# Performance work log

Hardware: AMD Instinct MI355X
Metric: run time of the kernel (lower is better)

Reference implementation:

```python
import jax, jax.numpy as jnp
import numpy as np

B, D, H, T = 256, 1024, 1024, 100
EPS = 1e-5  # torch LayerNorm default

def _ln(x, g, b):
    m = jnp.mean(x, axis=-1, keepdims=True)
    v = jnp.mean((x - m) ** 2, axis=-1, keepdims=True)
    return (x - m) * jax.lax.rsqrt(v + EPS) * g + b

def _gru_cell(x, h, Wih, Whh, bih, bhh):
    # PyTorch GRUCell math. Wih:[3H,in], Whh:[3H,H], gate order r,z,n.
    gi = x @ Wih.T + bih
    gh = h @ Whh.T + bhh
    ir, iz, inn = jnp.split(gi, 3, axis=-1)
    hr, hz, hn = jnp.split(gh, 3, axis=-1)
    r = jax.nn.sigmoid(ir + hr)
    z = jax.nn.sigmoid(iz + hz)
    n = jnp.tanh(inn + r * hn)
    return (1.0 - z) * n + z * h

def setup_inputs() -> dict:
    key = jax.random.key(0)
    ks = jax.random.split(key, 16)
    def xav(k, shape):
        fan_out, fan_in = shape
        lim = np.sqrt(6.0 / (fan_in + fan_out))
        return jax.random.uniform(k, shape, jnp.float32, -lim, lim)
    inp = {
        'x': jax.random.normal(ks[0], (B, D), jnp.float32),
        'enc_W1': xav(ks[1], (H, D)), 'enc_b1': jnp.zeros((H,), jnp.float32),
        'enc_ln1_g': jnp.ones((H,), jnp.float32), 'enc_ln1_b': jnp.zeros((H,), jnp.float32),
        'enc_W2': xav(ks[2], (H, H)), 'enc_b2': jnp.zeros((H,), jnp.float32),
        'enc_ln2_g': jnp.ones((H,), jnp.float32), 'enc_ln2_b': jnp.zeros((H,), jnp.float32),
        'gru_Wih0': jax.random.uniform(ks[3], (3 * H, H), jnp.float32, -1/np.sqrt(H), 1/np.sqrt(H)),
        'gru_Whh0': jax.random.uniform(ks[4], (3 * H, H), jnp.float32, -1/np.sqrt(H), 1/np.sqrt(H)),
        'gru_bih0': jnp.zeros((3 * H,), jnp.float32), 'gru_bhh0': jnp.zeros((3 * H,), jnp.float32),
        'gru_Wih1': jax.random.uniform(ks[5], (3 * H, H), jnp.float32, -1/np.sqrt(H), 1/np.sqrt(H)),
        'gru_Whh1': jax.random.uniform(ks[6], (3 * H, H), jnp.float32, -1/np.sqrt(H), 1/np.sqrt(H)),
        'gru_bih1': jnp.zeros((3 * H,), jnp.float32), 'gru_bhh1': jnp.zeros((3 * H,), jnp.float32),
        'hn_g': jnp.ones((H,), jnp.float32), 'hn_b': jnp.zeros((H,), jnp.float32),
        'proj_W1': xav(ks[7], (H, H)), 'proj_b1': jnp.zeros((H,), jnp.float32),
        'proj_ln_g': jnp.ones((H,), jnp.float32), 'proj_ln_b': jnp.zeros((H,), jnp.float32),
        'proj_W2': xav(ks[8], (D, H)), 'proj_b2': jnp.zeros((D,), jnp.float32),
        'max_length': T,
    }
    return inp

def reference(x, enc_W1, enc_b1, enc_ln1_g, enc_ln1_b, enc_W2, enc_b2, enc_ln2_g, enc_ln2_b,
              gru_Wih0, gru_Whh0, gru_bih0, gru_bhh0, gru_Wih1, gru_Whh1, gru_bih1, gru_bhh1,
              hn_g, hn_b, proj_W1, proj_b1, proj_ln_g, proj_ln_b, proj_W2, proj_b2, max_length):
    # Encoder: Linear -> LN -> ReLU, twice
    e = jax.nn.relu(_ln(x @ enc_W1.T + enc_b1, enc_ln1_g, enc_ln1_b))
    e = jax.nn.relu(_ln(e @ enc_W2.T + enc_b2, enc_ln2_g, enc_ln2_b))
    h_init = jnp.zeros((2, x.shape[0], gru_Whh0.shape[1]), x.dtype)  # [num_layers,B,H]

    def step(carry, _):
        h, cur = carry
        hn = _ln(h, hn_g, hn_b)  # hidden_norm applied to h0 each step
        h0 = _gru_cell(cur, hn[0], gru_Wih0, gru_Whh0, gru_bih0, gru_bhh0)
        h1 = _gru_cell(h0, hn[1], gru_Wih1, gru_Whh1, gru_bih1, gru_bhh1)
        return (jnp.stack([h0, h1]), h1), h1

    (_, _), ys = jax.lax.scan(step, (h_init, e), None, length=max_length)
    outputs = jnp.transpose(ys, (1, 0, 2))  # [B,T,H]
    p = jax.nn.relu(_ln(outputs @ proj_W1.T + proj_b1, proj_ln_g, proj_ln_b))
    return p @ proj_W2.T + proj_b2  # [B,T,D]
```

## Files before the change

kernel.cpp:

```cpp
#include <hip/hip_runtime.h>
#include <stdint.h>

#define T_STEPS 100
#define Bb 256
#define Hh 1024
#define Dd 1024
#define BM 64
#define BN 64
#define BK 64

typedef _Float16 f16;
typedef _Float16 f16x8 __attribute__((ext_vector_type(8)));
typedef _Float16 f16x4 __attribute__((ext_vector_type(4)));
typedef float    f32x4 __attribute__((ext_vector_type(4)));

__global__ __launch_bounds__(256) void k_f32_split(const float* __restrict__ s,
                                                   f16* __restrict__ hi, f16* __restrict__ lo, int n) {
  int i = (blockIdx.x * blockDim.x + threadIdx.x) * 4;
  if (i >= n) return;
  float4 v = *(const float4*)(s + i);
  f16x4 h = { (f16)v.x, (f16)v.y, (f16)v.z, (f16)v.w };
  f16x4 L = { (f16)(v.x - (float)h.x), (f16)(v.y - (float)h.y),
              (f16)(v.z - (float)h.z), (f16)(v.w - (float)h.w) };
  *(f16x4*)(hi + i) = h;
  *(f16x4*)(lo + i) = L;
}

__global__ __launch_bounds__(256) void k_f32_to_f16(const float* __restrict__ s,
                                                    f16* __restrict__ d, int n) {
  int i = (blockIdx.x * blockDim.x + threadIdx.x) * 4;
  if (i >= n) return;
  float4 v = *(const float4*)(s + i);
  f16x4 o = { (f16)v.x, (f16)v.y, (f16)v.z, (f16)v.w };
  *(f16x4*)(d + i) = o;
}

__global__ __launch_bounds__(256) void k_init_hn(const float* __restrict__ lnb,
                                                 float* __restrict__ hn0f, float* __restrict__ hn1f,
                                                 f16* __restrict__ h0hi, f16* __restrict__ h0lo,
                                                 f16* __restrict__ h1hi, f16* __restrict__ h1lo) {
  int m = blockIdx.x, tid = threadIdx.x;
  for (int k = 0; k < 4; ++k) {
    int c = tid + k * 256;
    float v = lnb[c];
    f16 h = (f16)v; f16 L = (f16)(v - (float)h);
    size_t idx = (size_t)m * Hh + c;
    hn0f[idx] = v; hn1f[idx] = v;
    h0hi[idx] = h; h0lo[idx] = L;
    h1hi[idx] = h; h1lo[idx] = L;
  }
}

template <int NCH>
__device__ __forceinline__ void stage_rows(const f16* __restrict__ g, int r0, int k0,
                                           f16* sdst, int tid) {
#pragma unroll
  for (int i = 0; i < NCH; ++i) {
    int slot = i * 256 + tid;
    int row  = slot >> 3;
    int pkg  = slot & 7;
    int lg   = pkg ^ (row & 7);
    const f16* src = g + (size_t)(r0 + row) * 1024 + k0 + lg * 8;
    f16* dst = sdst + (size_t)slot * 8;
    __builtin_amdgcn_global_load_lds((const __attribute__((address_space(1))) void*)src,
                                     (__attribute__((address_space(3))) void*)dst, 16, 0, 0);
  }
}

#define FBM 64
#define FBN 96
__global__ __launch_bounds__(256) void k_gru_gemm(
    const f16* __restrict__ A0h, const f16* __restrict__ A0l,
    const f16* __restrict__ B0h, const f16* __restrict__ B0l, float* __restrict__ C0,
    const f16* __restrict__ A1h, const f16* __restrict__ A1l,
    const f16* __restrict__ B1h, const f16* __restrict__ B1l, float* __restrict__ C1) {
  const int wgid = blockIdx.x;
  const int xcd = wgid & 7, idx = wgid >> 3;
  const int bx = idx & 3, yp = (idx >> 2) & 3, bz = idx >> 4;
  const int by = xcd * 4 + yp;

  const f16* Ah = bz ? A1h : A0h;
  const f16* Al = bz ? A1l : A0l;
  const f16* Bh = bz ? B1h : B0h;
  const f16* Bl = bz ? B1l : B0l;
  float*     C  = bz ? C1  : C0;

  __shared__ alignas(16) f16 sAh[3][FBM * BK];
  __shared__ alignas(16) f16 sAl[3][FBM * BK];
  __shared__ alignas(16) f16 sBh[3][FBN * BK];
  __shared__ alignas(16) f16 sBl[3][FBN * BK];

  const int tid = threadIdx.x;
  const int w = tid >> 6, l = tid & 63;
  const int wr = w >> 1, wc = w & 1;
  const int lrow = l & 15, lkg = l >> 4;
  const int m0 = bx * FBM, n0 = by * FBN;

  f32x4 acc[2][3] = {};

#pragma unroll
  for (int pt = 0; pt < 3; ++pt) {
    stage_rows<2>(Ah, m0, pt * BK, sAh[pt], tid);
    stage_rows<2>(Al, m0, pt * BK, sAl[pt], tid);
    stage_rows<3>(Bh, n0, pt * BK, sBh[pt], tid);
    stage_rows<3>(Bl, n0, pt * BK, sBl[pt], tid);
  }

#pragma unroll
  for (int it = 0; it < 16; ++it) {
    const int cur = it % 3;
    if (it <= 13)      asm volatile("s_waitcnt vmcnt(20)" ::: "memory");
    else if (it == 14) asm volatile("s_waitcnt vmcnt(10)" ::: "memory");
    else               asm volatile("s_waitcnt vmcnt(0)" ::: "memory");
    __builtin_amdgcn_s_barrier();

    f16x8 ah[2][2], al[2][2], bh[2][3], bl[2][3];
#pragma unroll
    for (int ks = 0; ks < 2; ++ks) {
#pragma unroll
      for (int fi = 0; fi < 2; ++fi) {
        int row = wr * 32 + fi * 16 + lrow;
        int pkg = (ks * 4 + lkg) ^ (row & 7);
        ah[ks][fi] = *(const f16x8*)&sAh[cur][row * BK + pkg * 8];
        al[ks][fi] = *(const f16x8*)&sAl[cur][row * BK + pkg * 8];
      }
#pragma unroll
      for (int fj = 0; fj < 3; ++fj) {
        int row = wc * 48 + fj * 16 + lrow;
        int pkg = (ks * 4 + lkg) ^ (row & 7);
        bh[ks][fj] = *(const f16x8*)&sBh[cur][row * BK + pkg * 8];
        bl[ks][fj] = *(const f16x8*)&sBl[cur][row * BK + pkg * 8];
      }
    }
    asm volatile("s_waitcnt lgkmcnt(0)" ::: "memory");
    __builtin_amdgcn_s_barrier();

    if (it < 13) {
      const int k0 = (it + 3) * BK;
      stage_rows<2>(Ah, m0, k0, sAh[cur], tid);
      stage_rows<2>(Al, m0, k0, sAl[cur], tid);
      stage_rows<3>(Bh, n0, k0, sBh[cur], tid);
      stage_rows<3>(Bl, n0, k0, sBl[cur], tid);
    }

#pragma unroll
    for (int ks = 0; ks < 2; ++ks)
#pragma unroll
      for (int fi = 0; fi < 2; ++fi)
#pragma unroll
        for (int fj = 0; fj < 3; ++fj) {
          acc[fi][fj] = __builtin_amdgcn_mfma_f32_16x16x32_f16(ah[ks][fi], bh[ks][fj], acc[fi][fj], 0, 0, 0);
          acc[fi][fj] = __builtin_amdgcn_mfma_f32_16x16x32_f16(ah[ks][fi], bl[ks][fj], acc[fi][fj], 0, 0, 0);
          acc[fi][fj] = __builtin_amdgcn_mfma_f32_16x16x32_f16(al[ks][fi], bh[ks][fj], acc[fi][fj], 0, 0, 0);
        }
  }

#pragma unroll
  for (int fi = 0; fi < 2; ++fi)
#pragma unroll
    for (int fj = 0; fj < 3; ++fj)
#pragma unroll
      for (int r = 0; r < 4; ++r) {
        int row = m0 + wr * 32 + fi * 16 + lkg * 4 + r;
        int col = n0 + wc * 48 + fj * 16 + lrow;
        C[(size_t)row * 3072 + col] = acc[fi][fj][r];
      }
}

__global__ __launch_bounds__(256) void k_gemm_big(const f16* __restrict__ A, const f16* __restrict__ B,
                                                  float* __restrict__ C, const float* __restrict__ bias,
                                                  int N) {
  __shared__ alignas(16) f16 sA[2][128 * BK];
  __shared__ alignas(16) f16 sB[2][128 * BK];
  const int tid = threadIdx.x;
  const int w = tid >> 6, l = tid & 63;
  const int wr = w >> 1, wc = w & 1;
  const int lrow = l & 15, lkg = l >> 4;
  const int m0 = blockIdx.x * 128, n0 = blockIdx.y * 128;

  f32x4 acc[4][4] = {};
  stage_rows<4>(A, m0, 0, sA[0], tid);
  stage_rows<4>(B, n0, 0, sB[0], tid);

  for (int it = 0; it < 16; ++it) {
    __syncthreads();
    const int cur = it & 1;
    if (it < 15) {
      const int k0 = (it + 1) * BK;
      stage_rows<4>(A, m0, k0, sA[cur ^ 1], tid);
      stage_rows<4>(B, n0, k0, sB[cur ^ 1], tid);
    }
#pragma unroll
    for (int ks = 0; ks < 2; ++ks) {
      f16x8 af[4], bf[4];
#pragma unroll
      for (int fi = 0; fi < 4; ++fi) {
        int row = wr * 64 + fi * 16 + lrow;
        int pkg = (ks * 4 + lkg) ^ (row & 7);
        af[fi] = *(const f16x8*)&sA[cur][row * BK + pkg * 8];
      }
#pragma unroll
      for (int fj = 0; fj < 4; ++fj) {
        int row = wc * 64 + fj * 16 + lrow;
        int pkg = (ks * 4 + lkg) ^ (row & 7);
        bf[fj] = *(const f16x8*)&sB[cur][row * BK + pkg * 8];
      }
#pragma unroll
      for (int fi = 0; fi < 4; ++fi)
#pragma unroll
        for (int fj = 0; fj < 4; ++fj)
          acc[fi][fj] = __builtin_amdgcn_mfma_f32_16x16x32_f16(af[fi], bf[fj], acc[fi][fj], 0, 0, 0);
    }
  }
#pragma unroll
  for (int fi = 0; fi < 4; ++fi)
#pragma unroll
    for (int fj = 0; fj < 4; ++fj)
#pragma unroll
      for (int r = 0; r < 4; ++r) {
        int row = m0 + wr * 64 + fi * 16 + lkg * 4 + r;
        int col = n0 + wc * 64 + fj * 16 + lrow;
        C[(size_t)row * N + col] = acc[fi][fj][r] + bias[col];
      }
}

__device__ __forceinline__ void stage_tile(const f16* __restrict__ g, int r0, int k0,
                                           f16* sdst, int tid) {
  stage_rows<2>(g, r0, k0, sdst, tid);
}

__global__ __launch_bounds__(256) void k_gemm3(const f16* __restrict__ Ah, const f16* __restrict__ Al,
                                               const f16* __restrict__ Bh, const f16* __restrict__ Bl,
                                               float* __restrict__ C, const float* __restrict__ bias,
                                               int N) {
  __shared__ alignas(16) f16 sA[2][BM * BK];
  __shared__ alignas(16) f16 sB[2][BN * BK];
  const int tid = threadIdx.x;
  const int w = tid >> 6, l = tid & 63;
  const int wr = w >> 1, wc = w & 1;
  const int lrow = l & 15, lkg = l >> 4;
  const int m0 = blockIdx.x * BM, n0 = blockIdx.y * BN;
  const int TOT = 48;

  f32x4 acc[2][2] = {};
  stage_tile(Ah, m0, 0, sA[0], tid);
  stage_tile(Bh, n0, 0, sB[0], tid);

  for (int it = 0; it < TOT; ++it) {
    __syncthreads();
    const int cur = it & 1;
    if (it + 1 < TOT) {
      const int nx = it + 1;
      const f16* An = (nx >= 32) ? Al : Ah;
      const f16* Bn = ((nx >> 4) == 1) ? Bl : Bh;
      const int k0 = (nx & 15) * BK;
      stage_tile(An, m0, k0, sA[cur ^ 1], tid);
      stage_tile(Bn, n0, k0, sB[cur ^ 1], tid);
    }
#pragma unroll
    for (int ks = 0; ks < 2; ++ks) {
      f16x8 af[2], bf[2];
#pragma unroll
      for (int fi = 0; fi < 2; ++fi) {
        int row = wr * 32 + fi * 16 + lrow;
        int pkg = (ks * 4 + lkg) ^ (row & 7);
        af[fi] = *(const f16x8*)&sA[cur][row * BK + pkg * 8];
      }
#pragma unroll
      for (int fj = 0; fj < 2; ++fj) {
        int row = wc * 32 + fj * 16 + lrow;
        int pkg = (ks * 4 + lkg) ^ (row & 7);
        bf[fj] = *(const f16x8*)&sB[cur][row * BK + pkg * 8];
      }
#pragma unroll
      for (int fi = 0; fi < 2; ++fi)
#pragma unroll
        for (int fj = 0; fj < 2; ++fj)
          acc[fi][fj] = __builtin_amdgcn_mfma_f32_16x16x32_f16(af[fi], bf[fj], acc[fi][fj], 0, 0, 0);
    }
  }
#pragma unroll
  for (int fi = 0; fi < 2; ++fi)
#pragma unroll
    for (int fj = 0; fj < 2; ++fj)
#pragma unroll
      for (int r = 0; r < 4; ++r) {
        int row = m0 + wr * 32 + fi * 16 + lkg * 4 + r;
        int col = n0 + wc * 32 + fj * 16 + lrow;
        C[(size_t)row * N + col] = acc[fi][fj][r] + (bias ? bias[col] : 0.f);
      }
}

__device__ __forceinline__ void block_sum2(float& a, float& b) {
#pragma unroll
  for (int o = 32; o > 0; o >>= 1) { a += __shfl_down(a, o, 64); b += __shfl_down(b, o, 64); }
  __shared__ float sa[4], sb[4];
  int w = threadIdx.x >> 6, l = threadIdx.x & 63;
  if (l == 0) { sa[w] = a; sb[w] = b; }
  __syncthreads();
  a = sa[0] + sa[1] + sa[2] + sa[3];
  b = sb[0] + sb[1] + sb[2] + sb[3];
}

__device__ __forceinline__ void split_store(float v, f16* hi, f16* lo, size_t idx) {
  f16 h = (f16)v;
  hi[idx] = h;
  lo[idx] = (f16)(v - (float)h);
}

__global__ __launch_bounds__(256) void k_gru_gate(const float* __restrict__ gi, const float* __restrict__ gh,
                                                  float* __restrict__ hnf,
                                                  f16* __restrict__ hnhi, f16* __restrict__ hnlo,
                                                  f16* __restrict__ xhi, f16* __restrict__ xlo,
                                                  const float* __restrict__ bih, const float* __restrict__ bhh,
                                                  const float* __restrict__ lng, const float* __restrict__ lnb,
                                                  f16* __restrict__ outp, long ostride) {
  int m = blockIdx.x, tid = threadIdx.x;
  float h[4];
  float s1 = 0.f, s2 = 0.f;
#pragma unroll
  for (int k = 0; k < 4; ++k) {
    int c = tid + k * 256;
    size_t g0 = (size_t)m * (3 * Hh) + c;
    float rr  = (gi[g0]          + bih[c])          + (gh[g0]          + bhh[c]);
    float zz  = (gi[g0 + Hh]     + bih[Hh + c])     + (gh[g0 + Hh]     + bhh[Hh + c]);
    float in_ =  gi[g0 + 2 * Hh] + bih[2 * Hh + c];
    float hn_ =  gh[g0 + 2 * Hh] + bhh[2 * Hh + c];
    float r = 1.f / (1.f + expf(-rr));
    float z = 1.f / (1.f + expf(-zz));
    float n = tanhf(in_ + r * hn_);
    float hp = hnf[(size_t)m * Hh + c];
    float hv = (1.f - z) * n + z * hp;
    h[k] = hv;
    split_store(hv, xhi, xlo, (size_t)m * Hh + c);
    if (outp) outp[(size_t)m * ostride + c] = (f16)hv;
    s1 += hv; s2 += hv * hv;
  }
  block_sum2(s1, s2);
  float mean = s1 * (1.f / Hh);
  float var  = s2 * (1.f / Hh) - mean * mean;
  float rs   = rsqrtf(var + 1e-5f);
#pragma unroll
  for (int k = 0; k < 4; ++k) {
    int c = tid + k * 256;
    float v = (h[k] - mean) * rs * lng[c] + lnb[c];
    hnf[(size_t)m * Hh + c] = v;
    split_store(v, hnhi, hnlo, (size_t)m * Hh + c);
  }
}

__global__ __launch_bounds__(256) void k_ln_relu(const float* __restrict__ pre,
                                                 const float* __restrict__ g, const float* __restrict__ b,
                                                 f16* __restrict__ hi, f16* __restrict__ lo) {
  int m = blockIdx.x, tid = threadIdx.x;
  float v[4]; float s1 = 0.f, s2 = 0.f;
#pragma unroll
  for (int k = 0; k < 4; ++k) {
    int c = tid + k * 256;
    float x = pre[(size_t)m * Hh + c];
    v[k] = x; s1 += x; s2 += x * x;
  }
  block_sum2(s1, s2);
  float mean = s1 * (1.f / Hh);
  float var  = s2 * (1.f / Hh) - mean * mean;
  float rs   = rsqrtf(var + 1e-5f);
#pragma unroll
  for (int k = 0; k < 4; ++k) {
    int c = tid + k * 256;
    float y = (v[k] - mean) * rs * g[c] + b[c];
    y = y > 0.f ? y : 0.f;
    f16 hh = (f16)y;
    hi[(size_t)m * Hh + c] = hh;
    if (lo) lo[(size_t)m * Hh + c] = (f16)(y - (float)hh);
  }
}

extern "C" void kernel_launch(void* const* d_in, const int* in_sizes, int n_in,
                              void* d_out, int out_size, void* d_ws, size_t ws_size,
                              hipStream_t stream) {
  (void)in_sizes; (void)n_in; (void)out_size; (void)ws_size;
  const float* x     = (const float*)d_in[0];
  const float* encW1 = (const float*)d_in[1];
  const float* encb1 = (const float*)d_in[2];
  const float* ln1g  = (const float*)d_in[3];
  const float* ln1b  = (const float*)d_in[4];
  const float* encW2 = (const float*)d_in[5];
  const float* encb2 = (const float*)d_in[6];
  const float* ln2g  = (const float*)d_in[7];
  const float* ln2b  = (const float*)d_in[8];
  const float* Wih0  = (const float*)d_in[9];
  const float* Whh0  = (const float*)d_in[10];
  const float* bih0  = (const float*)d_in[11];
  const float* bhh0  = (const float*)d_in[12];
  const float* Wih1  = (const float*)d_in[13];
  const float* Whh1  = (const float*)d_in[14];
  const float* bih1  = (const float*)d_in[15];
  const float* bhh1  = (const float*)d_in[16];
  const float* hng   = (const float*)d_in[17];
  const float* hnb   = (const float*)d_in[18];
  const float* pW1   = (const float*)d_in[19];
  const float* pb1   = (const float*)d_in[20];
  const float* plng  = (const float*)d_in[21];
  const float* plnb  = (const float*)d_in[22];
  const float* pW2   = (const float*)d_in[23];
  const float* pb2   = (const float*)d_in[24];

  char* p = (char*)d_ws;
  auto alloc = [&](size_t bytes) { void* r = (void*)p; p += (bytes + 255) & ~(size_t)255; return r; };
  auto fpair = [&](size_t n, f16** hi, f16** lo) {
    *hi = (f16*)alloc(n * 2); *lo = (f16*)alloc(n * 2);
  };
  f16 *We1h, *We1l, *We2h, *We2l, *Wih0h, *Wih0l, *Whh0h, *Whh0l, *Wih1h, *Wih1l, *Whh1h, *Whh1l;
  fpair((size_t)Hh * Dd, &We1h, &We1l);
  fpair((size_t)Hh * Hh, &We2h, &We2l);
  fpair((size_t)3 * Hh * Hh, &Wih0h, &Wih0l);
  fpair((size_t)3 * Hh * Hh, &Whh0h, &Whh0l);
  fpair((size_t)3 * Hh * Hh, &Wih1h, &Wih1l);
  fpair((size_t)3 * Hh * Hh, &Whh1h, &Whh1l);
  f16* pW1h = (f16*)alloc((size_t)Hh * Hh * 2);
  f16* pW2h = (f16*)alloc((size_t)Dd * Hh * 2);
  f16 *xhi, *xlo, *curh, *curl, *x1h, *x1l, *hn0h, *hn0l, *hn1h, *hn1l;
  fpair((size_t)Bb * Dd, &xhi, &xlo);
  fpair((size_t)Bb * Hh, &curh, &curl);
  fpair((size_t)Bb * Hh, &x1h, &x1l);
  fpair((size_t)Bb * Hh, &hn0h, &hn0l);
  fpair((size_t)Bb * Hh, &hn1h, &hn1l);
  float* hn0f = (float*)alloc((size_t)Bb * Hh * 4);
  float* hn1f = (float*)alloc((size_t)Bb * Hh * 4);
  float* gif  = (float*)alloc((size_t)Bb * 3 * Hh * 4);
  float* ghf  = (float*)alloc((size_t)Bb * 3 * Hh * 4);
  f16* outsh  = (f16*)alloc((size_t)Bb * T_STEPS * Hh * 2);
  f16* ph     = outsh;
  float* pre  = (float*)d_out;

  auto spl = [&](const float* s, f16* hi, f16* lo, int n) {
    hipLaunchKernelGGL(k_f32_split, dim3((n / 4 + 255) / 256), dim3(256), 0, stream, s, hi, lo, n);
  };
  auto conv = [&](const float* s, f16* d, int n) {
    hipLaunchKernelGGL(k_f32_to_f16, dim3((n / 4 + 255) / 256), dim3(256), 0, stream, s, d, n);
  };
  spl(x, xhi, xlo, Bb * Dd);
  spl(encW1, We1h, We1l, Hh * Dd);
  spl(encW2, We2h, We2l, Hh * Hh);
  spl(Wih0, Wih0h, Wih0l, 3 * Hh * Hh);
  spl(Whh0, Whh0h, Whh0l, 3 * Hh * Hh);
  spl(Wih1, Wih1h, Wih1l, 3 * Hh * Hh);
  spl(Whh1, Whh1h, Whh1l, 3 * Hh * Hh);
  conv(pW1, pW1h, Hh * Hh);
  conv(pW2, pW2h, Dd * Hh);
  hipLaunchKernelGGL(k_init_hn, dim3(Bb), dim3(256), 0, stream, hnb, hn0f, hn1f, hn0h, hn0l, hn1h, hn1l);

  hipLaunchKernelGGL(k_gemm3, dim3(Bb / BM, Hh / BN), dim3(256), 0, stream,
                     xhi, xlo, We1h, We1l, gif, encb1, Hh);
  hipLaunchKernelGGL(k_ln_relu, dim3(Bb), dim3(256), 0, stream, gif, ln1g, ln1b, x1h, x1l);
  hipLaunchKernelGGL(k_gemm3, dim3(Bb / BM, Hh / BN), dim3(256), 0, stream,
                     x1h, x1l, We2h, We2l, gif, encb2, Hh);
  hipLaunchKernelGGL(k_ln_relu, dim3(Bb), dim3(256), 0, stream, gif, ln2g, ln2b, curh, curl);

  for (int t = 0; t < T_STEPS; ++t) {
    hipLaunchKernelGGL(k_gru_gemm, dim3(256), dim3(256), 0, stream,
                       curh, curl, Wih0h, Wih0l, gif, hn0h, hn0l, Whh0h, Whh0l, ghf);
    hipLaunchKernelGGL(k_gru_gate, dim3(Bb), dim3(256), 0, stream,
                       gif, ghf, hn0f, hn0h, hn0l, x1h, x1l, bih0, bhh0, hng, hnb,
                       (f16*)nullptr, (long)0);
    hipLaunchKernelGGL(k_gru_gemm, dim3(256), dim3(256), 0, stream,
                       x1h, x1l, Wih1h, Wih1l, gif, hn1h, hn1l, Whh1h, Whh1l, ghf);
    hipLaunchKernelGGL(k_gru_gate, dim3(Bb), dim3(256), 0, stream,
                       gif, ghf, hn1f, hn1h, hn1l, curh, curl, bih1, bhh1, hng, hnb,
                       outsh + (size_t)t * Hh, (long)T_STEPS * Hh);
  }

  hipLaunchKernelGGL(k_gemm_big, dim3(Bb * T_STEPS / 128, Hh / 128), dim3(256), 0, stream,
                     outsh, pW1h, pre, pb1, Hh);
  hipLaunchKernelGGL(k_ln_relu, dim3(Bb * T_STEPS), dim3(256), 0, stream, pre, plng, plnb,
                     ph, (f16*)nullptr);
  hipLaunchKernelGGL(k_gemm_big, dim3(Bb * T_STEPS / 128, Dd / 128), dim3(256), 0, stream,
                     ph, pW2h, (float*)d_out, pb2, Dd);
}
```

Before: 4.692 ms.

## Deepen GRU GEMM pipeline to six 32-wide K stages with one barrier

```diff
diff --git a/kernel.cpp b/kernel.cpp
--- a/kernel.cpp
+++ b/kernel.cpp
@@ -69,6 +69,27 @@
 
 #define FBM 64
 #define FBN 96
+
+__device__ __forceinline__ void stage32(const f16* __restrict__ Ah, const f16* __restrict__ Al,
+                                        const f16* __restrict__ Bh, const f16* __restrict__ Bl,
+                                        int m0, int n0, int k0,
+                                        f16* sAh, f16* sAl, f16* sBh, f16* sBl, int tid) {
+#pragma unroll
+  for (int i = 0; i < 5; ++i) {
+    int c = i * 256 + tid;
+    const f16* g; f16* s; int off, r0;
+    if (c < 512)      { g = (c < 256) ? Ah : Al; s = (c < 256) ? sAh : sAl; off = c & 255; r0 = m0; }
+    else              { int cb = c - 512;
+                        g = (cb < 384) ? Bh : Bl; s = (cb < 384) ? sBh : sBl;
+                        off = (cb >= 384) ? cb - 384 : cb; r0 = n0; }
+    int row = off >> 2, pkg = off & 3;
+    int lg  = pkg ^ ((row >> 1) & 3);
+    const f16* src = g + (size_t)(r0 + row) * 1024 + k0 + lg * 8;
+    __builtin_amdgcn_global_load_lds((const __attribute__((address_space(1))) void*)src,
+                                     (__attribute__((address_space(3))) void*)(s + off * 8), 16, 0, 0);
+  }
+}
+
 __global__ __launch_bounds__(256) void k_gru_gemm(
     const f16* __restrict__ A0h, const f16* __restrict__ A0l,
     const f16* __restrict__ B0h, const f16* __restrict__ B0l, float* __restrict__ C0,
@@ -85,10 +106,10 @@
   const f16* Bl = bz ? B1l : B0l;
   float*     C  = bz ? C1  : C0;
 
-  __shared__ alignas(16) f16 sAh[3][FBM * BK];
-  __shared__ alignas(16) f16 sAl[3][FBM * BK];
-  __shared__ alignas(16) f16 sBh[3][FBN * BK];
-  __shared__ alignas(16) f16 sBl[3][FBN * BK];
+  __shared__ alignas(16) f16 sAh[6][FBM * 32];
+  __shared__ alignas(16) f16 sAl[6][FBM * 32];
+  __shared__ alignas(16) f16 sBh[6][FBN * 32];
+  __shared__ alignas(16) f16 sBl[6][FBN * 32];
 
   const int tid = threadIdx.x;
   const int w = tid >> 6, l = tid & 63;
@@ -99,60 +120,58 @@
   f32x4 acc[2][3] = {};
 
 #pragma unroll
-  for (int pt = 0; pt < 3; ++pt) {
-    stage_rows<2>(Ah, m0, pt * BK, sAh[pt], tid);
-    stage_rows<2>(Al, m0, pt * BK, sAl[pt], tid);
-    stage_rows<3>(Bh, n0, pt * BK, sBh[pt], tid);
-    stage_rows<3>(Bl, n0, pt * BK, sBl[pt], tid);
-  }
-
-#pragma unroll
-  for (int it = 0; it < 16; ++it) {
-    const int cur = it % 3;
-    if (it <= 13)      asm volatile("s_waitcnt vmcnt(20)" ::: "memory");
-    else if (it == 14) asm volatile("s_waitcnt vmcnt(10)" ::: "memory");
-    else               asm volatile("s_waitcnt vmcnt(0)" ::: "memory");
+  for (int pt = 0; pt < 5; ++pt)
+    stage32(Ah, Al, Bh, Bl, m0, n0, pt * 32, sAh[pt], sAl[pt], sBh[pt], sBl[pt], tid);
+
+#pragma unroll
+  for (int j = 0; j < 32; ++j) {
+    const int buf = j % 6;
+    if (j <= 27)      asm volatile("s_waitcnt vmcnt(20)" ::: "memory");
+    else if (j == 28) asm volatile("s_waitcnt vmcnt(15)" ::: "memory");
+    else if (j == 29) asm volatile("s_waitcnt vmcnt(10)" ::: "memory");
+    else if (j == 30) asm volatile("s_waitcnt vmcnt(5)"  ::: "memory");
+    else              asm volatile("s_waitcnt vmcnt(0)"  ::: "memory");
     __builtin_amdgcn_s_barrier();
-
-    f16x8 ah[2][2], al[2][2], bh[2][3], bl[2][3];
-#pragma unroll
-    for (int ks = 0; ks < 2; ++ks) {
-#pragma unroll
-      for (int fi = 0; fi < 2; ++fi) {
-        int row = wr * 32 + fi * 16 + lrow;
-        int pkg = (ks * 4 + lkg) ^ (row & 7);
-        ah[ks][fi] = *(const f16x8*)&sAh[cur][row * BK + pkg * 8];
-        al[ks][fi] = *(const f16x8*)&sAl[cur][row * BK + pkg * 8];
-      }
-#pragma unroll
-      for (int fj = 0; fj < 3; ++fj) {
-        int row = wc * 48 + fj * 16 + lrow;
-        int pkg = (ks * 4 + lkg) ^ (row & 7);
-        bh[ks][fj] = *(const f16x8*)&sBh[cur][row * BK + pkg * 8];
-        bl[ks][fj] = *(const f16x8*)&sBl[cur][row * BK + pkg * 8];
-      }
-    }
-    asm volatile("s_waitcnt lgkmcnt(0)" ::: "memory");
-    __builtin_amdgcn_s_barrier();
-
-    if (it < 13) {
-      const int k0 = (it + 3) * BK;
-      stage_rows<2>(Ah, m0, k0, sAh[cur], tid);
-      stage_rows<2>(Al, m0, k0, sAl[cur], tid);
-      stage_rows<3>(Bh, n0, k0, sBh[cur], tid);
-      stage_rows<3>(Bl, n0, k0, sBl[cur], tid);
-    }
-
-#pragma unroll
-    for (int ks = 0; ks < 2; ++ks)
-#pragma unroll
-      for (int fi = 0; fi < 2; ++fi)
-#pragma unroll
-        for (int fj = 0; fj < 3; ++fj) {
-          acc[fi][fj] = __builtin_amdgcn_mfma_f32_16x16x32_f16(ah[ks][fi], bh[ks][fj], acc[fi][fj], 0, 0, 0);
-          acc[fi][fj] = __builtin_amdgcn_mfma_f32_16x16x32_f16(ah[ks][fi], bl[ks][fj], acc[fi][fj], 0, 0, 0);
-          acc[fi][fj] = __builtin_amdgcn_mfma_f32_16x16x32_f16(al[ks][fi], bh[ks][fj], acc[fi][fj], 0, 0, 0);
-        }
+    __builtin_amdgcn_sched_barrier(0);
+
+    if (j <= 26) {
+      const int sb = (j + 5) % 6;
+      stage32(Ah, Al, Bh, Bl, m0, n0, (j + 5) * 32, sAh[sb], sAl[sb], sBh[sb], sBl[sb], tid);
+    }
+
+    f16x8 ah[2], al[2], bh[3], bl[3];
+#pragma unroll
+    for (int fi = 0; fi < 2; ++fi) {
+      int row = wr * 32 + fi * 16 + lrow;
+      int pkg = lkg ^ ((row >> 1) & 3);
+      ah[fi] = *(const f16x8*)&sAh[buf][row * 32 + pkg * 8];
+      al[fi] = *(const f16x8*)&sAl[buf][row * 32 + pkg * 8];
+    }
+#pragma unroll
+    for (int fj = 0; fj < 3; ++fj) {
+      int row = wc * 48 + fj * 16 + lrow;
+      int pkg = lkg ^ ((row >> 1) & 3);
+      bh[fj] = *(const f16x8*)&sBh[buf][row * 32 + pkg * 8];
+      bl[fj] = *(const f16x8*)&sBl[buf][row * 32 + pkg * 8];
+    }
+
+    __builtin_amdgcn_s_setprio(1);
+#pragma unroll
+    for (int fi = 0; fi < 2; ++fi)
+#pragma unroll
+      for (int fj = 0; fj < 3; ++fj)
+        acc[fi][fj] = __builtin_amdgcn_mfma_f32_16x16x32_f16(ah[fi], bh[fj], acc[fi][fj], 0, 0, 0);
+#pragma unroll
+    for (int fi = 0; fi < 2; ++fi)
+#pragma unroll
+      for (int fj = 0; fj < 3; ++fj)
+        acc[fi][fj] = __builtin_amdgcn_mfma_f32_16x16x32_f16(ah[fi], bl[fj], acc[fi][fj], 0, 0, 0);
+#pragma unroll
+    for (int fi = 0; fi < 2; ++fi)
+#pragma unroll
+      for (int fj = 0; fj < 3; ++fj)
+        acc[fi][fj] = __builtin_amdgcn_mfma_f32_16x16x32_f16(al[fi], bh[fj], acc[fi][fj], 0, 0, 0);
+    __builtin_amdgcn_s_setprio(0);
   }
 
 #pragma unroll
```

Result: slower. 5.536 ms (+18.0%).

## Restructure GRU gate GEMM pipeline to single barrier with 2-ahead prefetch

Applied to the files above, without the earlier changes.

```diff
diff --git a/kernel.cpp b/kernel.cpp
--- a/kernel.cpp
+++ b/kernel.cpp
@@ -99,60 +99,55 @@
   f32x4 acc[2][3] = {};
 
 #pragma unroll
-  for (int pt = 0; pt < 3; ++pt) {
+  for (int pt = 0; pt < 2; ++pt) {
     stage_rows<2>(Ah, m0, pt * BK, sAh[pt], tid);
     stage_rows<2>(Al, m0, pt * BK, sAl[pt], tid);
     stage_rows<3>(Bh, n0, pt * BK, sBh[pt], tid);
     stage_rows<3>(Bl, n0, pt * BK, sBl[pt], tid);
   }
 
-#pragma unroll
-  for (int it = 0; it < 16; ++it) {
-    const int cur = it % 3;
-    if (it <= 13)      asm volatile("s_waitcnt vmcnt(20)" ::: "memory");
-    else if (it == 14) asm volatile("s_waitcnt vmcnt(10)" ::: "memory");
-    else               asm volatile("s_waitcnt vmcnt(0)" ::: "memory");
+  for (int j = 0; j < 16; ++j) {
+    const int buf = j % 3;
+    if (j < 15) asm volatile("s_waitcnt vmcnt(10)" ::: "memory");
+    else        asm volatile("s_waitcnt vmcnt(0)"  ::: "memory");
     __builtin_amdgcn_s_barrier();
-
-    f16x8 ah[2][2], al[2][2], bh[2][3], bl[2][3];
+    __builtin_amdgcn_sched_barrier(0);
+
+    if (j <= 13) {
+      const int sb = (j + 2) % 3;
+      const int k0 = (j + 2) * BK;
+      stage_rows<2>(Ah, m0, k0, sAh[sb], tid);
+      stage_rows<2>(Al, m0, k0, sAl[sb], tid);
+      stage_rows<3>(Bh, n0, k0, sBh[sb], tid);
+      stage_rows<3>(Bl, n0, k0, sBl[sb], tid);
+    }
+
 #pragma unroll
     for (int ks = 0; ks < 2; ++ks) {
+      f16x8 ah[2], al[2], bh[3], bl[3];
 #pragma unroll
       for (int fi = 0; fi < 2; ++fi) {
         int row = wr * 32 + fi * 16 + lrow;
         int pkg = (ks * 4 + lkg) ^ (row & 7);
-        ah[ks][fi] = *(const f16x8*)&sAh[cur][row * BK + pkg * 8];
-        al[ks][fi] = *(const f16x8*)&sAl[cur][row * BK + pkg * 8];
+        ah[fi] = *(const f16x8*)&sAh[buf][row * BK + pkg * 8];
+        al[fi] = *(const f16x8*)&sAl[buf][row * BK + pkg * 8];
       }
 #pragma unroll
       for (int fj = 0; fj < 3; ++fj) {
         int row = wc * 48 + fj * 16 + lrow;
         int pkg = (ks * 4 + lkg) ^ (row & 7);
-        bh[ks][fj] = *(const f16x8*)&sBh[cur][row * BK + pkg * 8];
-        bl[ks][fj] = *(const f16x8*)&sBl[cur][row * BK + pkg * 8];
-      }
-    }
-    asm volatile("s_waitcnt lgkmcnt(0)" ::: "memory");
-    __builtin_amdgcn_s_barrier();
-
-    if (it < 13) {
-      const int k0 = (it + 3) * BK;
-      stage_rows<2>(Ah, m0, k0, sAh[cur], tid);
-      stage_rows<2>(Al, m0, k0, sAl[cur], tid);
-      stage_rows<3>(Bh, n0, k0, sBh[cur], tid);
-      stage_rows<3>(Bl, n0, k0, sBl[cur], tid);
-    }
-
-#pragma unroll
-    for (int ks = 0; ks < 2; ++ks)
+        bh[fj] = *(const f16x8*)&sBh[buf][row * BK + pkg * 8];
+        bl[fj] = *(const f16x8*)&sBl[buf][row * BK + pkg * 8];
+      }
 #pragma unroll
       for (int fi = 0; fi < 2; ++fi)
 #pragma unroll
         for (int fj = 0; fj < 3; ++fj) {
-          acc[fi][fj] = __builtin_amdgcn_mfma_f32_16x16x32_f16(ah[ks][fi], bh[ks][fj], acc[fi][fj], 0, 0, 0);
-          acc[fi][fj] = __builtin_amdgcn_mfma_f32_16x16x32_f16(ah[ks][fi], bl[ks][fj], acc[fi][fj], 0, 0, 0);
-          acc[fi][fj] = __builtin_amdgcn_mfma_f32_16x16x32_f16(al[ks][fi], bh[ks][fj], acc[fi][fj], 0, 0, 0);
+          acc[fi][fj] = __builtin_amdgcn_mfma_f32_16x16x32_f16(ah[fi], bh[fj], acc[fi][fj], 0, 0, 0);
+          acc[fi][fj] = __builtin_amdgcn_mfma_f32_16x16x32_f16(ah[fi], bl[fj], acc[fi][fj], 0, 0, 0);
+          acc[fi][fj] = __builtin_amdgcn_mfma_f32_16x16x32_f16(al[fi], bh[fj], acc[fi][fj], 0, 0, 0);
         }
+    }
   }
 
 #pragma unroll
```

Result: slower. 6.931 ms (+47.7%).

## Shrink GRU GEMM tile to 32 rows with 128-thread blocks and double buffering

Applied to the files above, without the earlier changes.

```diff
diff --git a/kernel.cpp b/kernel.cpp
--- a/kernel.cpp
+++ b/kernel.cpp
@@ -51,12 +51,12 @@
   }
 }
 
-template <int NCH>
+template <int NCH, int NT>
 __device__ __forceinline__ void stage_rows(const f16* __restrict__ g, int r0, int k0,
                                            f16* sdst, int tid) {
 #pragma unroll
   for (int i = 0; i < NCH; ++i) {
-    int slot = i * 256 + tid;
+    int slot = i * NT + tid;
     int row  = slot >> 3;
     int pkg  = slot & 7;
     int lg   = pkg ^ (row & 7);
@@ -67,17 +67,20 @@
   }
 }
 
-#define FBM 64
+#define FBM 32
 #define FBN 96
-__global__ __launch_bounds__(256) void k_gru_gemm(
+__global__ __launch_bounds__(128) void k_gru_gemm(
     const f16* __restrict__ A0h, const f16* __restrict__ A0l,
     const f16* __restrict__ B0h, const f16* __restrict__ B0l, float* __restrict__ C0,
     const f16* __restrict__ A1h, const f16* __restrict__ A1l,
     const f16* __restrict__ B1h, const f16* __restrict__ B1l, float* __restrict__ C1) {
   const int wgid = blockIdx.x;
-  const int xcd = wgid & 7, idx = wgid >> 3;
-  const int bx = idx & 3, yp = (idx >> 2) & 3, bz = idx >> 4;
-  const int by = xcd * 4 + yp;
+  const int xcd = wgid & 7;
+  const int idx = wgid >> 3;
+  const int bx  = idx & 7;
+  const int yp  = (idx >> 3) & 3;
+  const int bz  = idx >> 5;
+  const int by  = xcd * 4 + yp;
 
   const f16* Ah = bz ? A1h : A0h;
   const f16* Al = bz ? A1l : A0l;
@@ -85,33 +88,31 @@
   const f16* Bl = bz ? B1l : B0l;
   float*     C  = bz ? C1  : C0;
 
-  __shared__ alignas(16) f16 sAh[3][FBM * BK];
-  __shared__ alignas(16) f16 sAl[3][FBM * BK];
-  __shared__ alignas(16) f16 sBh[3][FBN * BK];
-  __shared__ alignas(16) f16 sBl[3][FBN * BK];
+  __shared__ alignas(16) f16 sAh[2][FBM * BK];
+  __shared__ alignas(16) f16 sAl[2][FBM * BK];
+  __shared__ alignas(16) f16 sBh[2][FBN * BK];
+  __shared__ alignas(16) f16 sBl[2][FBN * BK];
 
   const int tid = threadIdx.x;
   const int w = tid >> 6, l = tid & 63;
-  const int wr = w >> 1, wc = w & 1;
   const int lrow = l & 15, lkg = l >> 4;
   const int m0 = bx * FBM, n0 = by * FBN;
 
   f32x4 acc[2][3] = {};
 
 #pragma unroll
-  for (int pt = 0; pt < 3; ++pt) {
-    stage_rows<2>(Ah, m0, pt * BK, sAh[pt], tid);
-    stage_rows<2>(Al, m0, pt * BK, sAl[pt], tid);
-    stage_rows<3>(Bh, n0, pt * BK, sBh[pt], tid);
-    stage_rows<3>(Bl, n0, pt * BK, sBl[pt], tid);
-  }
-
-#pragma unroll
-  for (int it = 0; it < 16; ++it) {
-    const int cur = it % 3;
-    if (it <= 13)      asm volatile("s_waitcnt vmcnt(20)" ::: "memory");
-    else if (it == 14) asm volatile("s_waitcnt vmcnt(10)" ::: "memory");
-    else               asm volatile("s_waitcnt vmcnt(0)" ::: "memory");
+  for (int pt = 0; pt < 2; ++pt) {
+    stage_rows<2, 128>(Ah, m0, pt * BK, sAh[pt], tid);
+    stage_rows<2, 128>(Al, m0, pt * BK, sAl[pt], tid);
+    stage_rows<6, 128>(Bh, n0, pt * BK, sBh[pt], tid);
+    stage_rows<6, 128>(Bl, n0, pt * BK, sBl[pt], tid);
+  }
+
+#pragma unroll
+  for (int j = 0; j < 16; ++j) {
+    const int buf = j & 1;
+    if (j < 15) asm volatile("s_waitcnt vmcnt(16)" ::: "memory");
+    else        asm volatile("s_waitcnt vmcnt(0)"  ::: "memory");
     __builtin_amdgcn_s_barrier();
 
     f16x8 ah[2][2], al[2][2], bh[2][3], bl[2][3];
@@ -119,28 +120,28 @@
     for (int ks = 0; ks < 2; ++ks) {
 #pragma unroll
       for (int fi = 0; fi < 2; ++fi) {
-        int row = wr * 32 + fi * 16 + lrow;
-        int pkg = (ks * 4 + lkg) ^ (row & 7);
-        ah[ks][fi] = *(const f16x8*)&sAh[cur][row * BK + pkg * 8];
-        al[ks][fi] = *(const f16x8*)&sAl[cur][row * BK + pkg * 8];
+        int row = fi * 16 + lrow;
+        int pkg = (ks * 4 + lkg) ^ (row & 7);
+        ah[ks][fi] = *(const f16x8*)&sAh[buf][row * BK + pkg * 8];
+        al[ks][fi] = *(const f16x8*)&sAl[buf][row * BK + pkg * 8];
       }
 #pragma unroll
       for (int fj = 0; fj < 3; ++fj) {
-        int row = wc * 48 + fj * 16 + lrow;
-        int pkg = (ks * 4 + lkg) ^ (row & 7);
-        bh[ks][fj] = *(const f16x8*)&sBh[cur][row * BK + pkg * 8];
-        bl[ks][fj] = *(const f16x8*)&sBl[cur][row * BK + pkg * 8];
+        int row = w * 48 + fj * 16 + lrow;
+        int pkg = (ks * 4 + lkg) ^ (row & 7);
+        bh[ks][fj] = *(const f16x8*)&sBh[buf][row * BK + pkg * 8];
+        bl[ks][fj] = *(const f16x8*)&sBl[buf][row * BK + pkg * 8];
       }
     }
     asm volatile("s_waitcnt lgkmcnt(0)" ::: "memory");
     __builtin_amdgcn_s_barrier();
 
-    if (it < 13) {
-      const int k0 = (it + 3) * BK;
-      stage_rows<2>(Ah, m0, k0, sAh[cur], tid);
-      stage_rows<2>(Al, m0, k0, sAl[cur], tid);
-      stage_rows<3>(Bh, n0, k0, sBh[cur], tid);
-      stage_rows<3>(Bl, n0, k0, sBl[cur], tid);
+    if (j <= 13) {
+      const int k0 = (j + 2) * BK;
+      stage_rows<2, 128>(Ah, m0, k0, sAh[buf], tid);
+      stage_rows<2, 128>(Al, m0, k0, sAl[buf], tid);
+      stage_rows<6, 128>(Bh, n0, k0, sBh[buf], tid);
+      stage_rows<6, 128>(Bl, n0, k0, sBl[buf], tid);
     }
 
 #pragma unroll
@@ -161,8 +162,8 @@
     for (int fj = 0; fj < 3; ++fj)
 #pragma unroll
       for (int r = 0; r < 4; ++r) {
-        int row = m0 + wr * 32 + fi * 16 + lkg * 4 + r;
-        int col = n0 + wc * 48 + fj * 16 + lrow;
+        int row = m0 + fi * 16 + lkg * 4 + r;
+        int col = n0 + w * 48 + fj * 16 + lrow;
         C[(size_t)row * 3072 + col] = acc[fi][fj][r];
       }
 }
@@ -179,16 +180,16 @@
   const int m0 = blockIdx.x * 128, n0 = blockIdx.y * 128;
 
   f32x4 acc[4][4] = {};
-  stage_rows<4>(A, m0, 0, sA[0], tid);
-  stage_rows<4>(B, n0, 0, sB[0], tid);
+  stage_rows<4, 256>(A, m0, 0, sA[0], tid);
+  stage_rows<4, 256>(B, n0, 0, sB[0], tid);
 
   for (int it = 0; it < 16; ++it) {
     __syncthreads();
     const int cur = it & 1;
     if (it < 15) {
       const int k0 = (it + 1) * BK;
-      stage_rows<4>(A, m0, k0, sA[cur ^ 1], tid);
-      stage_rows<4>(B, n0, k0, sB[cur ^ 1], tid);
+      stage_rows<4, 256>(A, m0, k0, sA[cur ^ 1], tid);
+      stage_rows<4, 256>(B, n0, k0, sB[cur ^ 1], tid);
     }
 #pragma unroll
     for (int ks = 0; ks < 2; ++ks) {
@@ -226,7 +227,7 @@
 
 __device__ __forceinline__ void stage_tile(const f16* __restrict__ g, int r0, int k0,
                                            f16* sdst, int tid) {
-  stage_rows<2>(g, r0, k0, sdst, tid);
+  stage_rows<2, 256>(g, r0, k0, sdst, tid);
 }
 
 __global__ __launch_bounds__(256) void k_gemm3(const f16* __restrict__ Ah, const f16* __restrict__ Al,
@@ -458,12 +459,12 @@
   hipLaunchKernelGGL(k_ln_relu, dim3(Bb), dim3(256), 0, stream, gif, ln2g, ln2b, curh, curl);
 
   for (int t = 0; t < T_STEPS; ++t) {
-    hipLaunchKernelGGL(k_gru_gemm, dim3(256), dim3(256), 0, stream,
+    hipLaunchKernelGGL(k_gru_gemm, dim3(512), dim3(128), 0, stream,
                        curh, curl, Wih0h, Wih0l, gif, hn0h, hn0l, Whh0h, Whh0l, ghf);
     hipLaunchKernelGGL(k_gru_gate, dim3(Bb), dim3(256), 0, stream,
                        gif, ghf, hn0f, hn0h, hn0l, x1h, x1l, bih0, bhh0, hng, hnb,
                        (f16*)nullptr, (long)0);
-    hipLaunchKernelGGL(k_gru_gemm, dim3(256), dim3(256), 0, stream,
+    hipLaunchKernelGGL(k_gru_gemm, dim3(512), dim3(128), 0, stream,
                        x1h, x1l, Wih1h, Wih1l, gif, hn1h, hn1l, Whh1h, Whh1l, ghf);
     hipLaunchKernelGGL(k_gru_gate, dim3(Bb), dim3(256), 0, stream,
                        gif, ghf, hn1f, hn1h, hn1l, curh, curl, bih1, bhh1, hng, hnb,
```

After: 4.914 ms. +4.7%, slower.
